# Performance work log

Hardware: AMD Instinct MI355X
Metric: run time of the kernel (lower is better)

Reference implementation:

```python
import jax, jax.numpy as jnp
import numpy as np

N = 50000   # nodes
E = 800000  # edges (before self-loops)
IN = 128; H = 4; C = 32; HC = H * C; OUT = 47
EPS = 1e-16  # PyG softmax denominator eps
NEG_SLOPE = 0.2


def setup_inputs() -> dict:
    key = jax.random.key(0)
    ks = jax.random.split(key, 20)
    g = lambda k, shape, s=0.1: (jax.random.normal(k, shape, dtype=jnp.float32) * s)
    inp = {}
    inp["x"] = jax.random.normal(ks[0], (N, IN), dtype=jnp.float32)
    inp["edge_index"] = jax.random.randint(ks[1], (2, E), 0, N, dtype=jnp.int32)
    # layer 0: GATConv(IN -> H*C, concat=True) + skip Linear(IN -> HC)
    inp["lin_w0"] = g(ks[2], (IN, HC)); inp["att_src0"] = g(ks[3], (H, C)); inp["att_dst0"] = g(ks[4], (H, C))
    inp["bias0"] = g(ks[5], (HC,)); inp["skip_w0"] = g(ks[6], (IN, HC)); inp["skip_b0"] = g(ks[7], (HC,))
    # layer 1: GATConv(HC -> H*C, concat=True) + skip Linear(HC -> HC)
    inp["lin_w1"] = g(ks[8], (HC, HC)); inp["att_src1"] = g(ks[9], (H, C)); inp["att_dst1"] = g(ks[10], (H, C))
    inp["bias1"] = g(ks[11], (HC,)); inp["skip_w1"] = g(ks[12], (HC, HC)); inp["skip_b1"] = g(ks[13], (HC,))
    # layer 2: GATConv(HC -> OUT, heads=H, concat=False) + skip Linear(HC -> OUT)
    inp["lin_w2"] = g(ks[14], (HC, H * OUT)); inp["att_src2"] = g(ks[15], (H, OUT)); inp["att_dst2"] = g(ks[16], (H, OUT))
    inp["bias2"] = g(ks[17], (OUT,)); inp["skip_w2"] = g(ks[18], (HC, OUT)); inp["skip_b2"] = g(ks[19], (OUT,))
    return inp


def _gat_conv(x, src, dst, lin_w, att_src, att_dst, bias, concat):
    """PyG GATConv (self-loops already appended to src/dst)."""
    h, c = att_src.shape
    n = x.shape[0]
    xh = (x @ lin_w).reshape(n, h, c)                      # [N, H, C]
    a_src = jnp.einsum('nhc,hc->nh', xh, att_src)          # [N, H]
    a_dst = jnp.einsum('nhc,hc->nh', xh, att_dst)          # [N, H]
    e = a_src[src] + a_dst[dst]                            # [E', H]
    e = jax.nn.leaky_relu(e, NEG_SLOPE)
    # segment softmax over incoming edges per destination node
    m = jax.ops.segment_max(e, dst, num_segments=n)        # [N, H]
    ex = jnp.exp(e - m[dst])
    s = jax.ops.segment_sum(ex, dst, num_segments=n)       # [N, H]
    alpha = ex / (s[dst] + EPS)                            # [E', H]
    out = jax.ops.segment_sum(xh[src] * alpha[:, :, None], dst, num_segments=n)  # [N, H, C]
    out = out.reshape(n, h * c) if concat else out.mean(axis=1)
    return out + bias


def reference(x, edge_index, lin_w0, att_src0, att_dst0, bias0, skip_w0, skip_b0,
              lin_w1, att_src1, att_dst1, bias1, skip_w1, skip_b1,
              lin_w2, att_src2, att_dst2, bias2, skip_w2, skip_b2):
    n = x.shape[0]
    loop = jnp.arange(n, dtype=edge_index.dtype)
    src = jnp.concatenate([edge_index[0], loop])
    dst = jnp.concatenate([edge_index[1], loop])
    # layer 0 (+ skip, ELU; dropout is identity at inference)
    x = _gat_conv(x, src, dst, lin_w0, att_src0, att_dst0, bias0, True) + x @ skip_w0 + skip_b0
    x = jax.nn.elu(x)
    # layer 1
    x = _gat_conv(x, src, dst, lin_w1, att_src1, att_dst1, bias1, True) + x @ skip_w1 + skip_b1
    x = jax.nn.elu(x)
    # layer 2 (concat=False -> head mean), no activation
    x = _gat_conv(x, src, dst, lin_w2, att_src2, att_dst2, bias2, False) + x @ skip_w2 + skip_b2
    return x
```

## Files before the change

### kernel.cpp

```cpp
#include <hip/hip_runtime.h>
#include <math.h>
#include <type_traits>

#define KD 128
#define HC 128
#define NF2 188
#define NF2PB 192
#define OUTC 47

typedef __attribute__((ext_vector_type(8))) __bf16 bf16x8;
typedef __attribute__((ext_vector_type(4))) float f32x4;
typedef __attribute__((ext_vector_type(2))) float f32x2;

#ifdef __has_builtin
#if __has_builtin(__builtin_amdgcn_cvt_pk_f32_fp8)
#define HAVE_CVT_FP8_DEC 1
#endif
#if __has_builtin(__builtin_amdgcn_cvt_pk_fp8_f32)
#define HAVE_CVT_FP8_ENC 1
#endif
#endif

__device__ inline float bfhi_to_f(unsigned int u) {
    union { unsigned int u; float f; } c; c.u = u & 0xFFFF0000u; return c.f;
}
__device__ inline float bflo_to_f(unsigned int u) {
    union { unsigned int u; float f; } c; c.u = u << 16; return c.f;
}
__device__ inline unsigned short f_to_bfu(float f) {
    return __builtin_bit_cast(unsigned short, (__bf16)f);
}
__device__ inline unsigned int pk_bf(float a, float b) {
    return (unsigned int)f_to_bfu(a) | ((unsigned int)f_to_bfu(b) << 16);
}

__device__ inline void dot2bf(float& acc, unsigned int x, unsigned int a) {
    asm("v_dot2_f32_bf16 %0, %1, %2, %0" : "+v"(acc) : "v"(x), "v"(a));
}
__device__ inline unsigned int permb(unsigned int hi, unsigned int lo, unsigned int sel) {
    return __builtin_amdgcn_perm(hi, lo, sel);
}

#ifndef HAVE_CVT_FP8_DEC
__device__ inline float fp8_to_f32_b(unsigned int b) {
    int e = (b >> 3) & 15, m = b & 7;
    float v = e ? ldexpf((float)(8 + m), e - 10) : ldexpf((float)m, -9);
    return (b & 0x80) ? -v : v;
}
#endif
__device__ inline void fp8x4_dec(unsigned int q, float& a, float& b, float& c, float& d) {
#ifdef HAVE_CVT_FP8_DEC
    f32x2 lo = __builtin_amdgcn_cvt_pk_f32_fp8((int)q, false);
    f32x2 hi = __builtin_amdgcn_cvt_pk_f32_fp8((int)q, true);
    a = lo[0]; b = lo[1]; c = hi[0]; d = hi[1];
#else
    a = fp8_to_f32_b(q & 0xFF); b = fp8_to_f32_b((q >> 8) & 0xFF);
    c = fp8_to_f32_b((q >> 16) & 0xFF); d = fp8_to_f32_b((q >> 24) & 0xFF);
#endif
}
__device__ inline unsigned char f32_to_fp8(float v) {
#ifdef HAVE_CVT_FP8_ENC
    return (unsigned char)(__builtin_amdgcn_cvt_pk_fp8_f32(v, v, 0, false) & 0xFF);
#else
    unsigned u = __builtin_bit_cast(unsigned, v);
    unsigned s = (u >> 24) & 0x80;
    float a = fabsf(v);
    if (a < 0.0009765625f) return (unsigned char)s;
    if (a >= 448.f) return (unsigned char)(s | 0x7E);
    int e; float m = frexpf(a, &e);
    int E = e - 1 + 7;
    int mi = (int)rintf(m * 16.f);
    if (mi == 16) { mi = 8; ++E; if (E >= 16) return (unsigned char)(s | 0x7E); }
    if (E <= 0) {
        int q = (int)rintf(a * 512.f); if (q > 7) q = 7;
        return (unsigned char)(s | q);
    }
    return (unsigned char)(s | (E << 3) | (mi - 8));
#endif
}
__device__ inline float fp8dot(unsigned int q, float4 al, float acc) {
    float a, b, c, d;
    fp8x4_dec(q, a, b, c, d);
    return acc + al.x * a + al.y * b + al.z * c + al.w * d;
}

#define NPART 8
#define EPB 2048

__global__ __launch_bounds__(256) void count_kernel(
    const int* __restrict__ dst, int* deg, int e, int rngsz) {
    int r = blockIdx.x & (NPART - 1);
    int chunk = blockIdx.x / NPART;
    int base = chunk * EPB + threadIdx.x * 8;
    int lo = r * rngsz, hi = lo + rngsz;
    if (base >= e) return;
    if (base + 7 < e) {
        int4 d0 = *(const int4*)(dst + base);
        int4 d1 = *(const int4*)(dst + base + 4);
        int dd[8] = {d0.x, d0.y, d0.z, d0.w, d1.x, d1.y, d1.z, d1.w};
#pragma unroll
        for (int k = 0; k < 8; ++k)
            if (dd[k] >= lo && dd[k] < hi) atomicAdd(&deg[dd[k]], 1);
    } else {
        for (int k = base; k < e; ++k) {
            int d = dst[k];
            if (d >= lo && d < hi) atomicAdd(&deg[d], 1);
        }
    }
}

__global__ __launch_bounds__(256) void scan_base_kernel(
    int* __restrict__ deg, int* counter,
    int* __restrict__ row_ptr, int* __restrict__ fill, int* __restrict__ col, int n) {
    int i = blockIdx.x * 256 + threadIdx.x;
    int v = (i < n) ? (deg[i] + 1) : 0;
    int lane = threadIdx.x & 63, w = threadIdx.x >> 6;
    int incl = v;
#pragma unroll
    for (int off = 1; off < 64; off <<= 1) {
        int u = __shfl_up(incl, off, 64);
        if (lane >= off) incl += u;
    }
    __shared__ int wsum[4];
    __shared__ int base_sh;
    if (lane == 63) wsum[w] = incl;
    __syncthreads();
    if (threadIdx.x == 0)
        base_sh = atomicAdd(counter, wsum[0] + wsum[1] + wsum[2] + wsum[3]);
    int woff = 0;
    for (int k = 0; k < w; ++k) woff += wsum[k];
    __syncthreads();
    int excl = base_sh + woff + incl - v;
    if (i < n) {
        row_ptr[i] = excl;
        col[excl] = i;
        fill[i] = excl + 1;
        deg[i] = v;
    }
}

__global__ __launch_bounds__(256) void fill_kernel(
    const int* __restrict__ ei, int* fill, int* col, int e, int rngsz) {
    int r = blockIdx.x & (NPART - 1);
    int chunk = blockIdx.x / NPART;
    int base = chunk * EPB + threadIdx.x * 8;
    int lo = r * rngsz, hi = lo + rngsz;
    if (base >= e) return;
    const int* dstp = ei + e;
    if (base + 7 < e) {
        int4 d0 = *(const int4*)(dstp + base);
        int4 d1 = *(const int4*)(dstp + base + 4);
        int dd[8] = {d0.x, d0.y, d0.z, d0.w, d1.x, d1.y, d1.z, d1.w};
#pragma unroll
        for (int k = 0; k < 8; ++k) {
            if (dd[k] >= lo && dd[k] < hi) {
                int pos = atomicAdd(&fill[dd[k]], 1);
                col[pos] = ei[base + k];
            }
        }
    } else {
        for (int k = base; k < e; ++k) {
            int d = dstp[k];
            if (d >= lo && d < hi) {
                int pos = atomicAdd(&fill[d], 1);
                col[pos] = ei[k];
            }
        }
    }
}

__global__ __launch_bounds__(256) void prep_w_kernel(
    const float* __restrict__ lw0, const float* __restrict__ sw0,
    const float* __restrict__ lw1, const float* __restrict__ sw1,
    const float* __restrict__ lw2, const float* __restrict__ sw2,
    __bf16* __restrict__ bt) {
    int idx = blockIdx.x * 256 + threadIdx.x;
    int buf = idx >> 15;
    int r = idx & 32767;
    int n = r >> 7, k = r & 127;
    float v = 0.f;
    if (buf == 0) v = (n < 128) ? lw0[k * 128 + n] : sw0[k * 128 + n - 128];
    else if (buf == 1) v = (n < 128) ? lw1[k * 128 + n] : sw1[k * 128 + n - 128];
    else {
        if (n < 188) v = lw2[k * 188 + n];
        else if (n >= 192 && n < 239) v = sw2[k * 47 + n - 192];
    }
    bt[idx] = (__bf16)v;
}

template <typename AT, typename SKT, int NLIN, int NSK, int TR>
__global__ __launch_bounds__(256) void gemm_fused_kernel(
    const AT* __restrict__ A, const __bf16* __restrict__ Bt,
    void* __restrict__ out0, int N0, int ldc0,
    const float* __restrict__ bias1, SKT* __restrict__ out1, int N1, int M) {
    __shared__ __bf16 As[64][136];
    __shared__ __bf16 Bs[64][136];
    int tid = threadIdx.x;
    int m0 = blockIdx.x * 64;

#pragma unroll
    for (int rep = 0; rep < 4; ++rep) {
        int idx = tid + rep * 256;
        int row = idx >> 4, seg = idx & 15;
        int gm = m0 + row;
        bf16x8 v = {};
        if (gm < M) {
            if constexpr (std::is_same<AT, float>::value) {
                const float* p = A + gm * KD + seg * 8;
                float4 f0 = *(const float4*)p;
                float4 f1 = *(const float4*)(p + 4);
                v[0] = (__bf16)f0.x; v[1] = (__bf16)f0.y; v[2] = (__bf16)f0.z; v[3] = (__bf16)f0.w;
                v[4] = (__bf16)f1.x; v[5] = (__bf16)f1.y; v[6] = (__bf16)f1.z; v[7] = (__bf16)f1.w;
            } else {
                v = *(const bf16x8*)(A + gm * KD + seg * 8);
            }
        }
        *(bf16x8*)&As[row][seg * 8] = v;
    }
    __syncthreads();

    int w = tid >> 6, lane = tid & 63;
    int lr = lane & 15, quad = lane >> 4;

#pragma unroll
    for (int t = 0; t < NLIN + NSK; ++t) {
        bool second = t >= NLIN;
        int N = second ? N1 : N0;
        int n0 = (second ? (t - NLIN) : t) * 64;
        if (t) __syncthreads();
#pragma unroll
        for (int rep = 0; rep < 4; ++rep) {
            int idx = tid + rep * 256;
            int row = idx >> 4, seg = idx & 15;
            *(bf16x8*)&Bs[row][seg * 8] =
                *(const bf16x8*)(Bt + ((t * 64 + row) << 7) + seg * 8);
        }
        __syncthreads();

        f32x4 acc[4] = {};
#pragma unroll
        for (int kc = 0; kc < 128; kc += 32) {
            bf16x8 a0 = *(const bf16x8*)&As[w * 16 + lr][kc + quad * 8];
            bf16x8 b0 = *(const bf16x8*)&Bs[lr][kc + quad * 8];
            bf16x8 b1 = *(const bf16x8*)&Bs[16 + lr][kc + quad * 8];
            bf16x8 b2 = *(const bf16x8*)&Bs[32 + lr][kc + quad * 8];
            bf16x8 b3 = *(const bf16x8*)&Bs[48 + lr][kc + quad * 8];
            acc[0] = __builtin_amdgcn_mfma_f32_16x16x32_bf16(a0, b0, acc[0], 0, 0, 0);
            acc[1] = __builtin_amdgcn_mfma_f32_16x16x32_bf16(a0, b1, acc[1], 0, 0, 0);
            acc[2] = __builtin_amdgcn_mfma_f32_16x16x32_bf16(a0, b2, acc[2], 0, 0, 0);
            acc[3] = __builtin_amdgcn_mfma_f32_16x16x32_bf16(a0, b3, acc[3], 0, 0, 0);
        }
#pragma unroll
        for (int c = 0; c < 4; ++c) {
#pragma unroll
            for (int reg = 0; reg < 4; ++reg) {
                int row = m0 + w * 16 + quad * 4 + reg;
                int colg = n0 + c * 16 + lr;
                if (row < M && colg < N) {
                    float v = acc[c][reg];
                    if (second) {
                        v += bias1[colg];
                        out1[row * N + colg] = (SKT)v;
                    } else if (TR) {
                        int h = (colg * 1395) >> 16;
                        ((unsigned char*)out0)[row * ldc0 + (colg - 47 * h) * 4 + h] =
                            f32_to_fp8(v);
                    } else {
                        ((__bf16*)out0)[row * ldc0 + colg] = (__bf16)v;
                    }
                }
            }
        }
    }
}

__global__ __launch_bounds__(256) void att_kernel(
    const __bf16* __restrict__ xh, const float* __restrict__ att_s,
    const float* __restrict__ att_d, float* __restrict__ a_src,
    float* __restrict__ a_dst, int n) {
    int tid = blockIdx.x * 256 + threadIdx.x;
    int node = tid >> 4;
    int l16 = threadIdx.x & 15;
    if (node >= n) return;
    uint4 q = ((const uint4*)xh)[node * 16 + l16];
    int f0 = l16 * 8;
    float4 as0 = *(const float4*)(att_s + f0);
    float4 as1 = *(const float4*)(att_s + f0 + 4);
    float4 ad0 = *(const float4*)(att_d + f0);
    float4 ad1 = *(const float4*)(att_d + f0 + 4);
    float x0 = bflo_to_f(q.x), x1 = bfhi_to_f(q.x);
    float x2 = bflo_to_f(q.y), x3 = bfhi_to_f(q.y);
    float x4 = bflo_to_f(q.z), x5 = bfhi_to_f(q.z);
    float x6 = bflo_to_f(q.w), x7 = bfhi_to_f(q.w);
    float hs = x0 * as0.x + x1 * as0.y + x2 * as0.z + x3 * as0.w
             + x4 * as1.x + x5 * as1.y + x6 * as1.z + x7 * as1.w;
    float hd = x0 * ad0.x + x1 * ad0.y + x2 * ad0.z + x3 * ad0.w
             + x4 * ad1.x + x5 * ad1.y + x6 * ad1.z + x7 * ad1.w;
    hs += __shfl_xor(hs, 1, 64); hs += __shfl_xor(hs, 2, 64);
    hd += __shfl_xor(hd, 1, 64); hd += __shfl_xor(hd, 2, 64);
    if ((l16 & 3) == 0) {
        int h = l16 >> 2;
        a_src[node * 4 + h] = hs;
        a_dst[node * 4 + h] = hd;
    }
}

__global__ __launch_bounds__(256) void att2_kernel(
    const unsigned char* __restrict__ xh8, const float* __restrict__ att_s,
    const float* __restrict__ att_d, float* __restrict__ a_src,
    float* __restrict__ a_dst, int n) {
    int node = (blockIdx.x * 256 + threadIdx.x) >> 6;
    int lane = threadIdx.x & 63;
    if (node >= n) return;
    float ps0 = 0.f, ps1 = 0.f, ps2 = 0.f, ps3 = 0.f;
    float pd0 = 0.f, pd1 = 0.f, pd2 = 0.f, pd3 = 0.f;
    if (lane < 47) {
        unsigned int q = ((const unsigned int*)(xh8 + node * NF2PB))[lane];
        float x0, x1, x2, x3;
        fp8x4_dec(q, x0, x1, x2, x3);
        ps0 = x0 * att_s[lane];       ps1 = x1 * att_s[47 + lane];
        ps2 = x2 * att_s[94 + lane];  ps3 = x3 * att_s[141 + lane];
        pd0 = x0 * att_d[lane];       pd1 = x1 * att_d[47 + lane];
        pd2 = x2 * att_d[94 + lane];  pd3 = x3 * att_d[141 + lane];
    }
#pragma unroll
    for (int off = 1; off <= 32; off <<= 1) {
        ps0 += __shfl_xor(ps0, off, 64); ps1 += __shfl_xor(ps1, off, 64);
        ps2 += __shfl_xor(ps2, off, 64); ps3 += __shfl_xor(ps3, off, 64);
        pd0 += __shfl_xor(pd0, off, 64); pd1 += __shfl_xor(pd1, off, 64);
        pd2 += __shfl_xor(pd2, off, 64); pd3 += __shfl_xor(pd3, off, 64);
    }
    if (lane < 4) {
        float vs = (lane == 0) ? ps0 : (lane == 1) ? ps1 : (lane == 2) ? ps2 : ps3;
        float vd = (lane == 0) ? pd0 : (lane == 1) ? pd1 : (lane == 2) ? pd2 : pd3;
        a_src[node * 4 + lane] = vs;
        a_dst[node * 4 + lane] = vd;
    }
}

template <int MODE>
__global__ __launch_bounds__(256) void agg_kernel(
    const void* __restrict__ xhp, const float* __restrict__ a_src,
    const float* __restrict__ a_dst, const void* __restrict__ skipp,
    const float* __restrict__ bias, const int* __restrict__ row_ptr,
    const int* __restrict__ deg, const int* __restrict__ col,
    void* __restrict__ outp, int n) {
    __shared__ float s_af[4][64][4];
    __shared__ unsigned s_ap[4][32][4];
    __shared__ int s_j[4][64];
    int w = threadIdx.x >> 6;
    int lane = threadIdx.x & 63;
    int node = (blockIdx.x << 2) + w;
    bool active = node < n;
    int node_c = active ? node : 0;
    int start = row_ptr[node_c];
    int end = start + (active ? deg[node_c] : 0);
    float4 ad4 = *(const float4*)(a_dst + 4 * node_c);
    float adh[4] = {ad4.x, ad4.y, ad4.z, ad4.w};

    int e0 = start + lane;
    bool ok0 = e0 < end;
    int jcap = ok0 ? col[e0] : 0;
    float evc[4];
    {
        float4 as4 = *(const float4*)(a_src + 4 * jcap);
        float v0 = as4.x + adh[0]; v0 = v0 > 0.f ? v0 : 0.2f * v0;
        float v1 = as4.y + adh[1]; v1 = v1 > 0.f ? v1 : 0.2f * v1;
        float v2 = as4.z + adh[2]; v2 = v2 > 0.f ? v2 : 0.2f * v2;
        float v3 = as4.w + adh[3]; v3 = v3 > 0.f ? v3 : 0.2f * v3;
        evc[0] = ok0 ? __expf(v0) : 0.f;
        evc[1] = ok0 ? __expf(v1) : 0.f;
        evc[2] = ok0 ? __expf(v2) : 0.f;
        evc[3] = ok0 ? __expf(v3) : 0.f;
    }
    float s[4] = {evc[0], evc[1], evc[2], evc[3]};
    for (int e = e0 + 64; e < end; e += 64) {
        int j = col[e];
        float4 as4 = *(const float4*)(a_src + 4 * j);
        float ev[4] = {as4.x + adh[0], as4.y + adh[1], as4.z + adh[2], as4.w + adh[3]};
#pragma unroll
        for (int h = 0; h < 4; ++h) {
            float v = ev[h] > 0.f ? ev[h] : 0.2f * ev[h];
            s[h] += __expf(v);
        }
    }
#pragma unroll
    for (int off = 32; off >= 1; off >>= 1)
#pragma unroll
        for (int h = 0; h < 4; ++h) s[h] += __shfl_xor(s[h], off, 64);
    float inv[4];
#pragma unroll
    for (int h = 0; h < 4; ++h) inv[h] = 1.f / (s[h] + 1e-16f);

    int half = lane >> 5, fl = lane & 31, myh2 = fl >> 3;
    bool lv = lane < 47;
    float acc0 = 0.f, acc1 = 0.f, acc2 = 0.f, acc3 = 0.f;
    const uint2* xb2 = (const uint2*)xhp;
    const unsigned int* x8 = (const unsigned int*)xhp;

    auto run_chunk = [&](int cnt) {
        if constexpr (MODE == 0) {
            int npair = (cnt + 1) >> 1;
            int p = half;
            for (; p + 2 < npair; p += 4) {
                int2 j0 = *(const int2*)&s_j[w][2 * p];
                int2 j1 = *(const int2*)&s_j[w][2 * p + 4];
                unsigned ap0 = s_ap[w][p][myh2];
                unsigned ap1 = s_ap[w][p + 2][myh2];
                uint2 qa0 = xb2[(j0.x << 5) + fl];
                uint2 qb0 = xb2[(j0.y << 5) + fl];
                uint2 qa1 = xb2[(j1.x << 5) + fl];
                uint2 qb1 = xb2[(j1.y << 5) + fl];
                dot2bf(acc0, permb(qb0.x, qa0.x, 0x05040100u), ap0);
                dot2bf(acc1, permb(qb0.x, qa0.x, 0x07060302u), ap0);
                dot2bf(acc2, permb(qb0.y, qa0.y, 0x05040100u), ap0);
                dot2bf(acc3, permb(qb0.y, qa0.y, 0x07060302u), ap0);
                dot2bf(acc0, permb(qb1.x, qa1.x, 0x05040100u), ap1);
                dot2bf(acc1, permb(qb1.x, qa1.x, 0x07060302u), ap1);
                dot2bf(acc2, permb(qb1.y, qa1.y, 0x05040100u), ap1);
                dot2bf(acc3, permb(qb1.y, qa1.y, 0x07060302u), ap1);
            }
            for (; p < npair; p += 2) {
                int2 j0 = *(const int2*)&s_j[w][2 * p];
                unsigned ap0 = s_ap[w][p][myh2];
                uint2 qa0 = xb2[(j0.x << 5) + fl];
                uint2 qb0 = xb2[(j0.y << 5) + fl];
                dot2bf(acc0, permb(qb0.x, qa0.x, 0x05040100u), ap0);
                dot2bf(acc1, permb(qb0.x, qa0.x, 0x07060302u), ap0);
                dot2bf(acc2, permb(qb0.y, qa0.y, 0x05040100u), ap0);
                dot2bf(acc3, permb(qb0.y, qa0.y, 0x07060302u), ap0);
            }
        } else {
            int t = 0;
            for (; t + 7 < cnt; t += 8) {
                unsigned int q0 = lv ? x8[s_j[w][t] * 48 + lane] : 0u;
                unsigned int q1 = lv ? x8[s_j[w][t + 1] * 48 + lane] : 0u;
                unsigned int q2 = lv ? x8[s_j[w][t + 2] * 48 + lane] : 0u;
                unsigned int q3 = lv ? x8[s_j[w][t + 3] * 48 + lane] : 0u;
                unsigned int q4 = lv ? x8[s_j[w][t + 4] * 48 + lane] : 0u;
                unsigned int q5 = lv ? x8[s_j[w][t + 5] * 48 + lane] : 0u;
                unsigned int q6 = lv ? x8[s_j[w][t + 6] * 48 + lane] : 0u;
                unsigned int q7 = lv ? x8[s_j[w][t + 7] * 48 + lane] : 0u;
                acc0 = fp8dot(q0, *(const float4*)&s_af[w][t][0], acc0);
                acc0 = fp8dot(q1, *(const float4*)&s_af[w][t + 1][0], acc0);
                acc0 = fp8dot(q2, *(const float4*)&s_af[w][t + 2][0], acc0);
                acc0 = fp8dot(q3, *(const float4*)&s_af[w][t + 3][0], acc0);
                acc0 = fp8dot(q4, *(const float4*)&s_af[w][t + 4][0], acc0);
                acc0 = fp8dot(q5, *(const float4*)&s_af[w][t + 5][0], acc0);
                acc0 = fp8dot(q6, *(const float4*)&s_af[w][t + 6][0], acc0);
                acc0 = fp8dot(q7, *(const float4*)&s_af[w][t + 7][0], acc0);
            }
            for (; t + 3 < cnt; t += 4) {
                unsigned int q0 = lv ? x8[s_j[w][t] * 48 + lane] : 0u;
                unsigned int q1 = lv ? x8[s_j[w][t + 1] * 48 + lane] : 0u;
                unsigned int q2 = lv ? x8[s_j[w][t + 2] * 48 + lane] : 0u;
                unsigned int q3 = lv ? x8[s_j[w][t + 3] * 48 + lane] : 0u;
                acc0 = fp8dot(q0, *(const float4*)&s_af[w][t][0], acc0);
                acc0 = fp8dot(q1, *(const float4*)&s_af[w][t + 1][0], acc0);
                acc0 = fp8dot(q2, *(const float4*)&s_af[w][t + 2][0], acc0);
                acc0 = fp8dot(q3, *(const float4*)&s_af[w][t + 3][0], acc0);
            }
            for (; t < cnt; ++t) {
                unsigned int q = lv ? x8[s_j[w][t] * 48 + lane] : 0u;
                acc0 = fp8dot(q, *(const float4*)&s_af[w][t][0], acc0);
            }
        }
    };

    {
        float al[4];
#pragma unroll
        for (int h = 0; h < 4; ++h) al[h] = evc[h] * inv[h];
        s_j[w][lane] = jcap;
        if constexpr (MODE == 0) {
            float o0 = __shfl_xor(al[0], 1, 64);
            float o1 = __shfl_xor(al[1], 1, 64);
            float o2 = __shfl_xor(al[2], 1, 64);
            float o3 = __shfl_xor(al[3], 1, 64);
            if (!(lane & 1)) {
                uint4 pk = make_uint4(pk_bf(al[0], o0), pk_bf(al[1], o1),
                                      pk_bf(al[2], o2), pk_bf(al[3], o3));
                *(uint4*)&s_ap[w][lane >> 1][0] = pk;
            }
        } else {
            *(float4*)&s_af[w][lane][0] = make_float4(al[0], al[1], al[2], al[3]);
        }
        int cnt = end - start; if (cnt > 64) cnt = 64;
        run_chunk(cnt);
    }
    for (int base = start + 64; base < end; base += 64) {
        int e = base + lane;
        bool ok = e < end;
        int jv = ok ? col[e] : 0;
        float4 as4 = *(const float4*)(a_src + 4 * jv);
        float asv[4] = {as4.x, as4.y, as4.z, as4.w};
        float al[4];
#pragma unroll
        for (int h = 0; h < 4; ++h) {
            float ev = asv[h] + adh[h];
            ev = ev > 0.f ? ev : 0.2f * ev;
            al[h] = ok ? __expf(ev) * inv[h] : 0.f;
        }
        s_j[w][lane] = jv;
        if constexpr (MODE == 0) {
            float o0 = __shfl_xor(al[0], 1, 64);
            float o1 = __shfl_xor(al[1], 1, 64);
            float o2 = __shfl_xor(al[2], 1, 64);
            float o3 = __shfl_xor(al[3], 1, 64);
            if (!(lane & 1)) {
                uint4 pk = make_uint4(pk_bf(al[0], o0), pk_bf(al[1], o1),
                                      pk_bf(al[2], o2), pk_bf(al[3], o3));
                *(uint4*)&s_ap[w][lane >> 1][0] = pk;
            }
        } else {
            *(float4*)&s_af[w][lane][0] = make_float4(al[0], al[1], al[2], al[3]);
        }
        int cnt = end - base; if (cnt > 64) cnt = 64;
        run_chunk(cnt);
    }

    if constexpr (MODE == 0) {
        acc0 += __shfl_xor(acc0, 32, 64);
        acc1 += __shfl_xor(acc1, 32, 64);
        acc2 += __shfl_xor(acc2, 32, 64);
        acc3 += __shfl_xor(acc3, 32, 64);
        if (active && half == 0) {
            float4 bb = *(const float4*)(bias + 4 * fl);
            uint2 skq = ((const uint2*)skipp)[(node << 5) + fl];
            float v0 = acc0 + bb.x + bflo_to_f(skq.x);
            float v1 = acc1 + bb.y + bfhi_to_f(skq.x);
            float v2 = acc2 + bb.z + bflo_to_f(skq.y);
            float v3 = acc3 + bb.w + bfhi_to_f(skq.y);
            v0 = v0 > 0.f ? v0 : (__expf(v0) - 1.f);
            v1 = v1 > 0.f ? v1 : (__expf(v1) - 1.f);
            v2 = v2 > 0.f ? v2 : (__expf(v2) - 1.f);
            v3 = v3 > 0.f ? v3 : (__expf(v3) - 1.f);
            uint2 o = make_uint2(pk_bf(v0, v1), pk_bf(v2, v3));
            ((uint2*)outp)[(node << 5) + fl] = o;
        }
    } else {
        if (active && lane < OUTC) {
            const float* skip = (const float*)skipp;
            float v = acc0 * 0.25f + bias[lane] + skip[node * OUTC + lane];
            ((float*)outp)[node * OUTC + lane] = v;
        }
    }
}

extern "C" void kernel_launch(void* const* d_in, const int* in_sizes, int n_in,
                              void* d_out, int out_size, void* d_ws, size_t ws_size,
                              hipStream_t stream) {
    const float* x        = (const float*)d_in[0];
    const int*   ei       = (const int*)d_in[1];
    const float* lin_w0   = (const float*)d_in[2];
    const float* att_src0 = (const float*)d_in[3];
    const float* att_dst0 = (const float*)d_in[4];
    const float* bias0    = (const float*)d_in[5];
    const float* skip_w0  = (const float*)d_in[6];
    const float* skip_b0  = (const float*)d_in[7];
    const float* lin_w1   = (const float*)d_in[8];
    const float* att_src1 = (const float*)d_in[9];
    const float* att_dst1 = (const float*)d_in[10];
    const float* bias1    = (const float*)d_in[11];
    const float* skip_w1  = (const float*)d_in[12];
    const float* skip_b1  = (const float*)d_in[13];
    const float* lin_w2   = (const float*)d_in[14];
    const float* att_src2 = (const float*)d_in[15];
    const float* att_dst2 = (const float*)d_in[16];
    const float* bias2    = (const float*)d_in[17];
    const float* skip_w2  = (const float*)d_in[18];
    const float* skip_b2  = (const float*)d_in[19];
    float* out = (float*)d_out;

    const int N = in_sizes[0] / KD;
    const int E = in_sizes[1] / 2;
    const int ET_ = E + N;

    char* ws = (char*)d_ws;
    size_t off = 0;
    auto alloc = [&](size_t bytes) -> void* {
        void* p = ws + off;
        off = (off + bytes + 255) & ~(size_t)255;
        return p;
    };
    void*   xh      = alloc((size_t)N * HC * 2 + 256);
    __bf16* buf_bf  = (__bf16*)alloc((size_t)N * HC * 2);
    void*   skipbuf = alloc((size_t)N * HC * 4);
    float* a_src    = (float*)alloc((size_t)N * 4 * 4);
    float* a_dst    = (float*)alloc((size_t)N * 4 * 4);
    int* deg        = (int*)alloc((size_t)N * 4);
    int* row_ptr    = (int*)alloc((size_t)N * 4);
    int* fill       = (int*)alloc((size_t)N * 4);
    int* col        = (int*)alloc((size_t)ET_ * 4);
    int* counter    = (int*)alloc(256);
    __bf16* Bt      = (__bf16*)alloc((size_t)3 * 256 * 128 * 2);

    prep_w_kernel<<<384, 256, 0, stream>>>(lin_w0, skip_w0, lin_w1, skip_w1,
                                           lin_w2, skip_w2, Bt);

    hipMemsetAsync(deg, 0, (size_t)N * 4, stream);
    hipMemsetAsync(counter, 0, 4, stream);
    int rngsz = (N + NPART - 1) / NPART;
    int cblocks = ((E + EPB - 1) / EPB) * NPART;
    count_kernel<<<cblocks, 256, 0, stream>>>(ei + E, deg, E, rngsz);
    scan_base_kernel<<<(N + 255) / 256, 256, 0, stream>>>(deg, counter, row_ptr, fill, col, N);
    fill_kernel<<<cblocks, 256, 0, stream>>>(ei, fill, col, E, rngsz);

    dim3 blk(256);
    int mblocks = (N + 63) / 64;
    int wave_blocks = (N + 3) / 4;
    int att_blocks = (N * 16 + 255) / 256;

    gemm_fused_kernel<float, __bf16, 2, 2, 0><<<mblocks, blk, 0, stream>>>(
        x, Bt, xh, HC, HC, skip_b0, (__bf16*)skipbuf, HC, N);
    att_kernel<<<att_blocks, blk, 0, stream>>>((const __bf16*)xh, att_src0, att_dst0,
                                               a_src, a_dst, N);
    agg_kernel<0><<<wave_blocks, blk, 0, stream>>>(xh, a_src, a_dst, skipbuf, bias0,
                                                   row_ptr, deg, col, buf_bf, N);
    gemm_fused_kernel<__bf16, __bf16, 2, 2, 0><<<mblocks, blk, 0, stream>>>(
        buf_bf, Bt + 32768, xh, HC, HC, skip_b1, (__bf16*)skipbuf, HC, N);
    att_kernel<<<att_blocks, blk, 0, stream>>>((const __bf16*)xh, att_src1, att_dst1,
                                               a_src, a_dst, N);
    agg_kernel<0><<<wave_blocks, blk, 0, stream>>>(xh, a_src, a_dst, skipbuf, bias1,
                                                   row_ptr, deg, col, buf_bf, N);
    gemm_fused_kernel<__bf16, float, 3, 1, 1><<<mblocks, blk, 0, stream>>>(
        buf_bf, Bt + 65536, xh, NF2, NF2PB, skip_b2, (float*)skipbuf, OUTC, N);
    att2_kernel<<<wave_blocks, blk, 0, stream>>>((const unsigned char*)xh, att_src2,
                                                 att_dst2, a_src, a_dst, N);
    agg_kernel<1><<<wave_blocks, blk, 0, stream>>>(xh, a_src, a_dst, skipbuf, bias2,
                                                   row_ptr, deg, col, out, N);
}
```

Before: 392.5 us.

## Aggregate layers 0-1 with 16-lane groups per node and 16-byte gathers

The bf16 aggregation for the first two GAT layers now assigns a 16-lane group to each destination node (16 nodes per block) instead of a full 64-lane wave. Each lane gathers 16 bytes (8 channels) per neighbour row. The softmax exponentials for the first two 16-edge chunks are kept in registers so they are not recomputed. This targets the wasted lanes and shuffle overhead of whole-wave processing at an average degree of about 17, in exchange for more iterations on high-degree nodes and more registers. The fp8 layer-2 path is split out into its own kernel with unchanged logic.

```diff
diff --git a/kernel.cpp b/kernel.cpp
--- a/kernel.cpp
+++ b/kernel.cpp
@@ -338,15 +338,165 @@
     }
 }
 
-template <int MODE>
-__global__ __launch_bounds__(256) void agg_kernel(
-    const void* __restrict__ xhp, const float* __restrict__ a_src,
-    const float* __restrict__ a_dst, const void* __restrict__ skipp,
+__global__ __launch_bounds__(256) void agg0_kernel(
+    const uint4* __restrict__ xh, const float* __restrict__ a_src,
+    const float* __restrict__ a_dst, const uint4* __restrict__ skipb,
     const float* __restrict__ bias, const int* __restrict__ row_ptr,
     const int* __restrict__ deg, const int* __restrict__ col,
-    void* __restrict__ outp, int n) {
+    uint4* __restrict__ outp, int n) {
+    __shared__ int s_j[16][16];
+    __shared__ unsigned s_ap[16][8][4];
+    int grp = threadIdx.x >> 4;
+    int l16 = threadIdx.x & 15;
+    int node = (blockIdx.x << 4) + grp;
+    bool active = node < n;
+    int node_c = active ? node : 0;
+    int start = row_ptr[node_c];
+    int end = start + (active ? deg[node_c] : 0);
+    float4 ad4 = *(const float4*)(a_dst + 4 * node_c);
+
+    float s0 = 0.f, s1 = 0.f, s2 = 0.f, s3 = 0.f;
+    float e00 = 0.f, e01 = 0.f, e02 = 0.f, e03 = 0.f;
+    float e10 = 0.f, e11 = 0.f, e12 = 0.f, e13 = 0.f;
+    int jc0 = 0, jc1 = 0;
+    int c = 0;
+    for (int base = start; base < end; base += 16, ++c) {
+        int e = base + l16;
+        bool ok = e < end;
+        int j = ok ? col[e] : 0;
+        float4 as4 = *(const float4*)(a_src + 4 * j);
+        float v0 = as4.x + ad4.x; v0 = v0 > 0.f ? v0 : 0.2f * v0;
+        float v1 = as4.y + ad4.y; v1 = v1 > 0.f ? v1 : 0.2f * v1;
+        float v2 = as4.z + ad4.z; v2 = v2 > 0.f ? v2 : 0.2f * v2;
+        float v3 = as4.w + ad4.w; v3 = v3 > 0.f ? v3 : 0.2f * v3;
+        float x0 = ok ? __expf(v0) : 0.f;
+        float x1 = ok ? __expf(v1) : 0.f;
+        float x2 = ok ? __expf(v2) : 0.f;
+        float x3 = ok ? __expf(v3) : 0.f;
+        s0 += x0; s1 += x1; s2 += x2; s3 += x3;
+        if (c == 0) { jc0 = j; e00 = x0; e01 = x1; e02 = x2; e03 = x3; }
+        else if (c == 1) { jc1 = j; e10 = x0; e11 = x1; e12 = x2; e13 = x3; }
+    }
+#pragma unroll
+    for (int off = 1; off <= 8; off <<= 1) {
+        s0 += __shfl_xor(s0, off, 64);
+        s1 += __shfl_xor(s1, off, 64);
+        s2 += __shfl_xor(s2, off, 64);
+        s3 += __shfl_xor(s3, off, 64);
+    }
+    float i0 = 1.f / (s0 + 1e-16f), i1 = 1.f / (s1 + 1e-16f);
+    float i2 = 1.f / (s2 + 1e-16f), i3 = 1.f / (s3 + 1e-16f);
+
+    int myh = l16 >> 2;
+    float a0 = 0.f, a1 = 0.f, a2 = 0.f, a3 = 0.f;
+    float a4 = 0.f, a5 = 0.f, a6 = 0.f, a7 = 0.f;
+    c = 0;
+    for (int base = start; base < end; base += 16, ++c) {
+        float al0, al1, al2, al3; int jv;
+        if (c == 0) {
+            jv = jc0; al0 = e00 * i0; al1 = e01 * i1; al2 = e02 * i2; al3 = e03 * i3;
+        } else if (c == 1) {
+            jv = jc1; al0 = e10 * i0; al1 = e11 * i1; al2 = e12 * i2; al3 = e13 * i3;
+        } else {
+            int e = base + l16;
+            bool ok = e < end;
+            jv = ok ? col[e] : 0;
+            float4 as4 = *(const float4*)(a_src + 4 * jv);
+            float v0 = as4.x + ad4.x; v0 = v0 > 0.f ? v0 : 0.2f * v0;
+            float v1 = as4.y + ad4.y; v1 = v1 > 0.f ? v1 : 0.2f * v1;
+            float v2 = as4.z + ad4.z; v2 = v2 > 0.f ? v2 : 0.2f * v2;
+            float v3 = as4.w + ad4.w; v3 = v3 > 0.f ? v3 : 0.2f * v3;
+            al0 = ok ? __expf(v0) * i0 : 0.f;
+            al1 = ok ? __expf(v1) * i1 : 0.f;
+            al2 = ok ? __expf(v2) * i2 : 0.f;
+            al3 = ok ? __expf(v3) * i3 : 0.f;
+        }
+        s_j[grp][l16] = jv;
+        float o0 = __shfl_xor(al0, 1, 64);
+        float o1 = __shfl_xor(al1, 1, 64);
+        float o2 = __shfl_xor(al2, 1, 64);
+        float o3 = __shfl_xor(al3, 1, 64);
+        if (!(l16 & 1)) {
+            *(uint4*)&s_ap[grp][l16 >> 1][0] =
+                make_uint4(pk_bf(al0, o0), pk_bf(al1, o1), pk_bf(al2, o2), pk_bf(al3, o3));
+        }
+        int cnt = end - base; if (cnt > 16) cnt = 16;
+        int npair = (cnt + 1) >> 1;
+        int p = 0;
+        for (; p + 1 < npair; p += 2) {
+            int2 jpa = *(const int2*)&s_j[grp][2 * p];
+            int2 jpb = *(const int2*)&s_j[grp][2 * p + 2];
+            unsigned apa = s_ap[grp][p][myh];
+            unsigned apb = s_ap[grp][p + 1][myh];
+            uint4 qa0 = xh[jpa.x * 16 + l16];
+            uint4 qb0 = xh[jpa.y * 16 + l16];
+            uint4 qa1 = xh[jpb.x * 16 + l16];
+            uint4 qb1 = xh[jpb.y * 16 + l16];
+            dot2bf(a0, permb(qb0.x, qa0.x, 0x05040100u), apa);
+            dot2bf(a1, permb(qb0.x, qa0.x, 0x07060302u), apa);
+            dot2bf(a2, permb(qb0.y, qa0.y, 0x05040100u), apa);
+            dot2bf(a3, permb(qb0.y, qa0.y, 0x07060302u), apa);
+            dot2bf(a4, permb(qb0.z, qa0.z, 0x05040100u), apa);
+            dot2bf(a5, permb(qb0.z, qa0.z, 0x07060302u), apa);
+            dot2bf(a6, permb(qb0.w, qa0.w, 0x05040100u), apa);
+            dot2bf(a7, permb(qb0.w, qa0.w, 0x07060302u), apa);
+            dot2bf(a0, permb(qb1.x, qa1.x, 0x05040100u), apb);
+            dot2bf(a1, permb(qb1.x, qa1.x, 0x07060302u), apb);
+            dot2bf(a2, permb(qb1.y, qa1.y, 0x05040100u), apb);
+            dot2bf(a3, permb(qb1.y, qa1.y, 0x07060302u), apb);
+            dot2bf(a4, permb(qb1.z, qa1.z, 0x05040100u), apb);
+            dot2bf(a5, permb(qb1.z, qa1.z, 0x07060302u), apb);
+            dot2bf(a6, permb(qb1.w, qa1.w, 0x05040100u), apb);
+            dot2bf(a7, permb(qb1.w, qa1.w, 0x07060302u), apb);
+        }
+        for (; p < npair; ++p) {
+            int2 jp = *(const int2*)&s_j[grp][2 * p];
+            unsigned ap = s_ap[grp][p][myh];
+            uint4 qa = xh[jp.x * 16 + l16];
+            uint4 qb = xh[jp.y * 16 + l16];
+            dot2bf(a0, permb(qb.x, qa.x, 0x05040100u), ap);
+            dot2bf(a1, permb(qb.x, qa.x, 0x07060302u), ap);
+            dot2bf(a2, permb(qb.y, qa.y, 0x05040100u), ap);
+            dot2bf(a3, permb(qb.y, qa.y, 0x07060302u), ap);
+            dot2bf(a4, permb(qb.z, qa.z, 0x05040100u), ap);
+            dot2bf(a5, permb(qb.z, qa.z, 0x07060302u), ap);
+            dot2bf(a6, permb(qb.w, qa.w, 0x05040100u), ap);
+            dot2bf(a7, permb(qb.w, qa.w, 0x07060302u), ap);
+        }
+    }
+
+    if (active) {
+        float4 b0 = *(const float4*)(bias + 8 * l16);
+        float4 b1 = *(const float4*)(bias + 8 * l16 + 4);
+        uint4 skq = skipb[node * 16 + l16];
+        float v0 = a0 + b0.x + bflo_to_f(skq.x);
+        float v1 = a1 + b0.y + bfhi_to_f(skq.x);
+        float v2 = a2 + b0.z + bflo_to_f(skq.y);
+        float v3 = a3 + b0.w + bfhi_to_f(skq.y);
+        float v4 = a4 + b1.x + bflo_to_f(skq.z);
+        float v5 = a5 + b1.y + bfhi_to_f(skq.z);
+        float v6 = a6 + b1.z + bflo_to_f(skq.w);
+        float v7 = a7 + b1.w + bfhi_to_f(skq.w);
+        v0 = v0 > 0.f ? v0 : (__expf(v0) - 1.f);
+        v1 = v1 > 0.f ? v1 : (__expf(v1) - 1.f);
+        v2 = v2 > 0.f ? v2 : (__expf(v2) - 1.f);
+        v3 = v3 > 0.f ? v3 : (__expf(v3) - 1.f);
+        v4 = v4 > 0.f ? v4 : (__expf(v4) - 1.f);
+        v5 = v5 > 0.f ? v5 : (__expf(v5) - 1.f);
+        v6 = v6 > 0.f ? v6 : (__expf(v6) - 1.f);
+        v7 = v7 > 0.f ? v7 : (__expf(v7) - 1.f);
+        outp[node * 16 + l16] =
+            make_uint4(pk_bf(v0, v1), pk_bf(v2, v3), pk_bf(v4, v5), pk_bf(v6, v7));
+    }
+}
+
+__global__ __launch_bounds__(256) void agg1_kernel(
+    const unsigned int* __restrict__ x8, const float* __restrict__ a_src,
+    const float* __restrict__ a_dst, const float* __restrict__ skip,
+    const float* __restrict__ bias, const int* __restrict__ row_ptr,
+    const int* __restrict__ deg, const int* __restrict__ col,
+    float* __restrict__ outp, int n) {
     __shared__ float s_af[4][64][4];
-    __shared__ unsigned s_ap[4][32][4];
     __shared__ int s_j[4][64];
     int w = threadIdx.x >> 6;
     int lane = threadIdx.x & 63;
@@ -392,78 +542,42 @@
 #pragma unroll
     for (int h = 0; h < 4; ++h) inv[h] = 1.f / (s[h] + 1e-16f);
 
-    int half = lane >> 5, fl = lane & 31, myh2 = fl >> 3;
     bool lv = lane < 47;
-    float acc0 = 0.f, acc1 = 0.f, acc2 = 0.f, acc3 = 0.f;
-    const uint2* xb2 = (const uint2*)xhp;
-    const unsigned int* x8 = (const unsigned int*)xhp;
+    float acc0 = 0.f;
 
     auto run_chunk = [&](int cnt) {
-        if constexpr (MODE == 0) {
-            int npair = (cnt + 1) >> 1;
-            int p = half;
-            for (; p + 2 < npair; p += 4) {
-                int2 j0 = *(const int2*)&s_j[w][2 * p];
-                int2 j1 = *(const int2*)&s_j[w][2 * p + 4];
-                unsigned ap0 = s_ap[w][p][myh2];
-                unsigned ap1 = s_ap[w][p + 2][myh2];
-                uint2 qa0 = xb2[(j0.x << 5) + fl];
-                uint2 qb0 = xb2[(j0.y << 5) + fl];
-                uint2 qa1 = xb2[(j1.x << 5) + fl];
-                uint2 qb1 = xb2[(j1.y << 5) + fl];
-                dot2bf(acc0, permb(qb0.x, qa0.x, 0x05040100u), ap0);
-                dot2bf(acc1, permb(qb0.x, qa0.x, 0x07060302u), ap0);
-                dot2bf(acc2, permb(qb0.y, qa0.y, 0x05040100u), ap0);
-                dot2bf(acc3, permb(qb0.y, qa0.y, 0x07060302u), ap0);
-                dot2bf(acc0, permb(qb1.x, qa1.x, 0x05040100u), ap1);
-                dot2bf(acc1, permb(qb1.x, qa1.x, 0x07060302u), ap1);
-                dot2bf(acc2, permb(qb1.y, qa1.y, 0x05040100u), ap1);
-                dot2bf(acc3, permb(qb1.y, qa1.y, 0x07060302u), ap1);
-            }
-            for (; p < npair; p += 2) {
-                int2 j0 = *(const int2*)&s_j[w][2 * p];
-                unsigned ap0 = s_ap[w][p][myh2];
-                uint2 qa0 = xb2[(j0.x << 5) + fl];
-                uint2 qb0 = xb2[(j0.y << 5) + fl];
-                dot2bf(acc0, permb(qb0.x, qa0.x, 0x05040100u), ap0);
-                dot2bf(acc1, permb(qb0.x, qa0.x, 0x07060302u), ap0);
-                dot2bf(acc2, permb(qb0.y, qa0.y, 0x05040100u), ap0);
-                dot2bf(acc3, permb(qb0.y, qa0.y, 0x07060302u), ap0);
-            }
-        } else {
-            int t = 0;
-            for (; t + 7 < cnt; t += 8) {
-                unsigned int q0 = lv ? x8[s_j[w][t] * 48 + lane] : 0u;
-                unsigned int q1 = lv ? x8[s_j[w][t + 1] * 48 + lane] : 0u;
-                unsigned int q2 = lv ? x8[s_j[w][t + 2] * 48 + lane] : 0u;
-                unsigned int q3 = lv ? x8[s_j[w][t + 3] * 48 + lane] : 0u;
-                unsigned int q4 = lv ? x8[s_j[w][t + 4] * 48 + lane] : 0u;
-                unsigned int q5 = lv ? x8[s_j[w][t + 5] * 48 + lane] : 0u;
-                unsigned int q6 = lv ? x8[s_j[w][t + 6] * 48 + lane] : 0u;
-                unsigned int q7 = lv ? x8[s_j[w][t + 7] * 48 + lane] : 0u;
-                acc0 = fp8dot(q0, *(const float4*)&s_af[w][t][0], acc0);
-                acc0 = fp8dot(q1, *(const float4*)&s_af[w][t + 1][0], acc0);
-                acc0 = fp8dot(q2, *(const float4*)&s_af[w][t + 2][0], acc0);
-                acc0 = fp8dot(q3, *(const float4*)&s_af[w][t + 3][0], acc0);
-                acc0 = fp8dot(q4, *(const float4*)&s_af[w][t + 4][0], acc0);
-                acc0 = fp8dot(q5, *(const float4*)&s_af[w][t + 5][0], acc0);
-                acc0 = fp8dot(q6, *(const float4*)&s_af[w][t + 6][0], acc0);
-                acc0 = fp8dot(q7, *(const float4*)&s_af[w][t + 7][0], acc0);
-            }
-            for (; t + 3 < cnt; t += 4) {
-                unsigned int q0 = lv ? x8[s_j[w][t] * 48 + lane] : 0u;
-                unsigned int q1 = lv ? x8[s_j[w][t + 1] * 48 + lane] : 0u;
-                unsigned int q2 = lv ? x8[s_j[w][t + 2] * 48 + lane] : 0u;
-                unsigned int q3 = lv ? x8[s_j[w][t + 3] * 48 + lane] : 0u;
-                acc0 = fp8dot(q0, *(const float4*)&s_af[w][t][0], acc0);
-                acc0 = fp8dot(q1, *(const float4*)&s_af[w][t + 1][0], acc0);
-                acc0 = fp8dot(q2, *(const float4*)&s_af[w][t + 2][0], acc0);
-                acc0 = fp8dot(q3, *(const float4*)&s_af[w][t + 3][0], acc0);
-            }
-            for (; t < cnt; ++t) {
-                unsigned int q = lv ? x8[s_j[w][t] * 48 + lane] : 0u;
-                acc0 = fp8dot(q, *(const float4*)&s_af[w][t][0], acc0);
-            }
+        int t = 0;
+        for (; t + 7 < cnt; t += 8) {
+            unsigned int q0 = lv ? x8[s_j[w][t] * 48 + lane] : 0u;
+            unsigned int q1 = lv ? x8[s_j[w][t + 1] * 48 + lane] : 0u;
+            unsigned int q2 = lv ? x8[s_j[w][t + 2] * 48 + lane] : 0u;
+            unsigned int q3 = lv ? x8[s_j[w][t + 3] * 48 + lane] : 0u;
+            unsigned int q4 = lv ? x8[s_j[w][t + 4] * 48 + lane] : 0u;
+            unsigned int q5 = lv ? x8[s_j[w][t + 5] * 48 + lane] : 0u;
+            unsigned int q6 = lv ? x8[s_j[w][t + 6] * 48 + lane] : 0u;
+            unsigned int q7 = lv ? x8[s_j[w][t + 7] * 48 + lane] : 0u;
+            acc0 = fp8dot(q0, *(const float4*)&s_af[w][t][0], acc0);
+            acc0 = fp8dot(q1, *(const float4*)&s_af[w][t + 1][0], acc0);
+            acc0 = fp8dot(q2, *(const float4*)&s_af[w][t + 2][0], acc0);
+            acc0 = fp8dot(q3, *(const float4*)&s_af[w][t + 3][0], acc0);
+            acc0 = fp8dot(q4, *(const float4*)&s_af[w][t + 4][0], acc0);
+            acc0 = fp8dot(q5, *(const float4*)&s_af[w][t + 5][0], acc0);
+            acc0 = fp8dot(q6, *(const float4*)&s_af[w][t + 6][0], acc0);
+            acc0 = fp8dot(q7, *(const float4*)&s_af[w][t + 7][0], acc0);
+        }
+        for (; t + 3 < cnt; t += 4) {
+            unsigned int q0 = lv ? x8[s_j[w][t] * 48 + lane] : 0u;
+            unsigned int q1 = lv ? x8[s_j[w][t + 1] * 48 + lane] : 0u;
+            unsigned int q2 = lv ? x8[s_j[w][t + 2] * 48 + lane] : 0u;
+            unsigned int q3 = lv ? x8[s_j[w][t + 3] * 48 + lane] : 0u;
+            acc0 = fp8dot(q0, *(const float4*)&s_af[w][t][0], acc0);
+            acc0 = fp8dot(q1, *(const float4*)&s_af[w][t + 1][0], acc0);
+            acc0 = fp8dot(q2, *(const float4*)&s_af[w][t + 2][0], acc0);
+            acc0 = fp8dot(q3, *(const float4*)&s_af[w][t + 3][0], acc0);
+        }
+        for (; t < cnt; ++t) {
+            unsigned int q = lv ? x8[s_j[w][t] * 48 + lane] : 0u;
+            acc0 = fp8dot(q, *(const float4*)&s_af[w][t][0], acc0);
         }
     };
 
@@ -472,19 +586,7 @@
 #pragma unroll
         for (int h = 0; h < 4; ++h) al[h] = evc[h] * inv[h];
         s_j[w][lane] = jcap;
-        if constexpr (MODE == 0) {
-            float o0 = __shfl_xor(al[0], 1, 64);
-            float o1 = __shfl_xor(al[1], 1, 64);
-            float o2 = __shfl_xor(al[2], 1, 64);
-            float o3 = __shfl_xor(al[3], 1, 64);
-            if (!(lane & 1)) {
-                uint4 pk = make_uint4(pk_bf(al[0], o0), pk_bf(al[1], o1),
-                                      pk_bf(al[2], o2), pk_bf(al[3], o3));
-                *(uint4*)&s_ap[w][lane >> 1][0] = pk;
-            }
-        } else {
-            *(float4*)&s_af[w][lane][0] = make_float4(al[0], al[1], al[2], al[3]);
-        }
+        *(float4*)&s_af[w][lane][0] = make_float4(al[0], al[1], al[2], al[3]);
         int cnt = end - start; if (cnt > 64) cnt = 64;
         run_chunk(cnt);
     }
@@ -493,57 +595,22 @@
         bool ok = e < end;
         int jv = ok ? col[e] : 0;
         float4 as4 = *(const float4*)(a_src + 4 * jv);
-        float asv[4] = {as4.x, as4.y, as4.z, as4.w};
         float al[4];
 #pragma unroll
         for (int h = 0; h < 4; ++h) {
-            float ev = asv[h] + adh[h];
+            float ev = ((const float*)&as4)[h] + adh[h];
             ev = ev > 0.f ? ev : 0.2f * ev;
             al[h] = ok ? __expf(ev) * inv[h] : 0.f;
         }
         s_j[w][lane] = jv;
-        if constexpr (MODE == 0) {
-            float o0 = __shfl_xor(al[0], 1, 64);
-            float o1 = __shfl_xor(al[1], 1, 64);
-            float o2 = __shfl_xor(al[2], 1, 64);
-            float o3 = __shfl_xor(al[3], 1, 64);
-            if (!(lane & 1)) {
-                uint4 pk = make_uint4(pk_bf(al[0], o0), pk_bf(al[1], o1),
-                                      pk_bf(al[2], o2), pk_bf(al[3], o3));
-                *(uint4*)&s_ap[w][lane >> 1][0] = pk;
-            }
-        } else {
-            *(float4*)&s_af[w][lane][0] = make_float4(al[0], al[1], al[2], al[3]);
-        }
+        *(float4*)&s_af[w][lane][0] = make_float4(al[0], al[1], al[2], al[3]);
         int cnt = end - base; if (cnt > 64) cnt = 64;
         run_chunk(cnt);
     }
 
-    if constexpr (MODE == 0) {
-        acc0 += __shfl_xor(acc0, 32, 64);
-        acc1 += __shfl_xor(acc1, 32, 64);
-        acc2 += __shfl_xor(acc2, 32, 64);
-        acc3 += __shfl_xor(acc3, 32, 64);
-        if (active && half == 0) {
-            float4 bb = *(const float4*)(bias + 4 * fl);
-            uint2 skq = ((const uint2*)skipp)[(node << 5) + fl];
-            float v0 = acc0 + bb.x + bflo_to_f(skq.x);
-            float v1 = acc1 + bb.y + bfhi_to_f(skq.x);
-            float v2 = acc2 + bb.z + bflo_to_f(skq.y);
-            float v3 = acc3 + bb.w + bfhi_to_f(skq.y);
-            v0 = v0 > 0.f ? v0 : (__expf(v0) - 1.f);
-            v1 = v1 > 0.f ? v1 : (__expf(v1) - 1.f);
-            v2 = v2 > 0.f ? v2 : (__expf(v2) - 1.f);
-            v3 = v3 > 0.f ? v3 : (__expf(v3) - 1.f);
-            uint2 o = make_uint2(pk_bf(v0, v1), pk_bf(v2, v3));
-            ((uint2*)outp)[(node << 5) + fl] = o;
-        }
-    } else {
-        if (active && lane < OUTC) {
-            const float* skip = (const float*)skipp;
-            float v = acc0 * 0.25f + bias[lane] + skip[node * OUTC + lane];
-            ((float*)outp)[node * OUTC + lane] = v;
-        }
+    if (active && lane < OUTC) {
+        float v = acc0 * 0.25f + bias[lane] + skip[node * OUTC + lane];
+        outp[node * OUTC + lane] = v;
     }
 }
 
@@ -609,24 +676,28 @@
     dim3 blk(256);
     int mblocks = (N + 63) / 64;
     int wave_blocks = (N + 3) / 4;
+    int grp_blocks = (N + 15) / 16;
     int att_blocks = (N * 16 + 255) / 256;
 
     gemm_fused_kernel<float, __bf16, 2, 2, 0><<<mblocks, blk, 0, stream>>>(
         x, Bt, xh, HC, HC, skip_b0, (__bf16*)skipbuf, HC, N);
     att_kernel<<<att_blocks, blk, 0, stream>>>((const __bf16*)xh, att_src0, att_dst0,
                                                a_src, a_dst, N);
-    agg_kernel<0><<<wave_blocks, blk, 0, stream>>>(xh, a_src, a_dst, skipbuf, bias0,
-                                                   row_ptr, deg, col, buf_bf, N);
+    agg0_kernel<<<grp_blocks, blk, 0, stream>>>((const uint4*)xh, a_src, a_dst,
+                                                (const uint4*)skipbuf, bias0,
+                                                row_ptr, deg, col, (uint4*)buf_bf, N);
     gemm_fused_kernel<__bf16, __bf16, 2, 2, 0><<<mblocks, blk, 0, stream>>>(
         buf_bf, Bt + 32768, xh, HC, HC, skip_b1, (__bf16*)skipbuf, HC, N);
     att_kernel<<<att_blocks, blk, 0, stream>>>((const __bf16*)xh, att_src1, att_dst1,
                                                a_src, a_dst, N);
-    agg_kernel<0><<<wave_blocks, blk, 0, stream>>>(xh, a_src, a_dst, skipbuf, bias1,
-                                                   row_ptr, deg, col, buf_bf, N);
+    agg0_kernel<<<grp_blocks, blk, 0, stream>>>((const uint4*)xh, a_src, a_dst,
+                                                (const uint4*)skipbuf, bias1,
+                                                row_ptr, deg, col, (uint4*)buf_bf, N);
     gemm_fused_kernel<__bf16, float, 3, 1, 1><<<mblocks, blk, 0, stream>>>(
         buf_bf, Bt + 65536, xh, NF2, NF2PB, skip_b2, (float*)skipbuf, OUTC, N);
     att2_kernel<<<wave_blocks, blk, 0, stream>>>((const unsigned char*)xh, att_src2,
                                                  att_dst2, a_src, a_dst, N);
-    agg_kernel<1><<<wave_blocks, blk, 0, stream>>>(xh, a_src, a_dst, skipbuf, bias2,
-                                                   row_ptr, deg, col, out, N);
-}
+    agg1_kernel<<<wave_blocks, blk, 0, stream>>>((const unsigned int*)xh, a_src, a_dst,
+                                                 (const float*)skipbuf, bias2,
+                                                 row_ptr, deg, col, out, N);
+}
```

Result: no change. 386.0 us, median of 2 (-1.7%).
